# Kernel tuning notes

Measured on AMD Instinct MI355X. Metric: run time of the kernel, lower is better.

Reference implementation:

```python
import jax, jax.numpy as jnp
import numpy as np

D_MODEL = 1024
D_HIDDEN = 32   # per-head MPS bond dimension
N_HEADS = 8
D_FF = 4096
EPS_LN = 1e-5
EPS_NORM = 1e-6


def layernorm(x, g, b):
    m = jnp.mean(x, axis=-1, keepdims=True)
    v = jnp.mean(jnp.square(x - m), axis=-1, keepdims=True)
    return (x - m) * jax.lax.rsqrt(v + EPS_LN) * g + b


def mps_recurrence(x, Wa, ba, h0, Wo, bo):
    # x: [B,S,D]. Per-token per-head transfer matrices A_t in R^{dh x dh}.
    B, S, D = x.shape
    A = (x @ Wa + ba).reshape(B, S, N_HEADS, D_HIDDEN, D_HIDDEN)
    A = jnp.moveaxis(A, 1, 0)  # [S,B,H,dh,dh]
    h_init = jnp.broadcast_to(h0, (B, N_HEADS, D_HIDDEN))  # [B,H,dh]

    def step(h, A_t):
        h = jnp.einsum('bhij,bhj->bhi', A_t, h)
        h = h / (jnp.linalg.norm(h, axis=-1, keepdims=True) + EPS_NORM)
        return h, h

    _, ys = jax.lax.scan(step, h_init, A)          # ys: [S,B,H,dh]
    ys = jnp.moveaxis(ys, 0, 1).reshape(B, S, N_HEADS * D_HIDDEN)
    return ys @ Wo + bo                            # [B,S,D]


def setup_inputs() -> dict:
    key = jax.random.key(0)
    ks = jax.random.split(key, 12)
    B, S, D = 4, 2048, D_MODEL
    inv = 1.0 / np.sqrt(D)
    inv_hd = 1.0 / np.sqrt(N_HEADS * D_HIDDEN)
    return {
        'x': jax.random.normal(ks[0], (B, S, D), jnp.float32),
        'ln1_g': jnp.ones((D,), jnp.float32),
        'ln1_b': jnp.zeros((D,), jnp.float32),
        'Wa': jax.random.normal(ks[1], (D, N_HEADS * D_HIDDEN * D_HIDDEN), jnp.float32) * inv,
        'ba': jnp.zeros((N_HEADS * D_HIDDEN * D_HIDDEN,), jnp.float32),
        'h0': jax.random.normal(ks[2], (N_HEADS, D_HIDDEN), jnp.float32) / np.sqrt(D_HIDDEN),
        'Wo': jax.random.normal(ks[3], (N_HEADS * D_HIDDEN, D), jnp.float32) * inv_hd,
        'bo': jnp.zeros((D,), jnp.float32),
        'ln2_g': jnp.ones((D,), jnp.float32),
        'ln2_b': jnp.zeros((D,), jnp.float32),
        'W1': jax.random.normal(ks[4], (D, D_FF), jnp.float32) * inv,
        'b1': jnp.zeros((D_FF,), jnp.float32),
        'W2': jax.random.normal(ks[5], (D_FF, D), jnp.float32) / np.sqrt(D_FF),
        'b2': jnp.zeros((D,), jnp.float32),
    }


def reference(x, ln1_g, ln1_b, Wa, ba, h0, Wo, bo, ln2_g, ln2_b, W1, b1, W2, b2):
    # Dropout in eval mode (identity).
    x = x + mps_recurrence(layernorm(x, ln1_g, ln1_b), Wa, ba, h0, Wo, bo)
    h = layernorm(x, ln2_g, ln2_b)
    ffn = jax.nn.gelu(h @ W1 + b1, approximate=False) @ W2 + b2
    return x + ffn
```

## Files before the change

### kernel.cpp

```cpp
#include <hip/hip_runtime.h>
#include <hip/hip_bf16.h>
#include <math.h>

typedef float f32x4 __attribute__((ext_vector_type(4)));
typedef __bf16 bf16x4 __attribute__((ext_vector_type(4)));
typedef __bf16 bf16x8 __attribute__((ext_vector_type(8)));

#define AS1(p) ((const __attribute__((address_space(1))) void*)(p))
#define AS3(p) ((__attribute__((address_space(3))) void*)(p))

static constexpr int D_MODEL = 1024;
static constexpr int S_LEN   = 2048;
static constexpr int BATCH   = 4;
static constexpr int NTOK    = BATCH * S_LEN;
static constexpr int NH      = 8;
static constexpr int DH      = 32;
static constexpr int NA      = NH * DH * DH;
static constexpr int D_FF    = 4096;
static constexpr int CHUNK   = 16;
static constexpr int NCHUNK  = S_LEN / CHUNK;

__device__ __forceinline__ void xcd_swizzle(int& bx, int& by) {
  int gx = gridDim.x;
  int orig = by * gx + bx;
  int r8 = orig & 7, j = orig >> 3;
  int bxn = j % gx, grp = j / gx;
  bx = bxn;
  by = grp * 8 + r8;
}

__device__ __forceinline__ float gelu_erf_fast(float v) {
  float z = fabsf(v) * 0.70710678118654752f;
  float t = __builtin_amdgcn_rcpf(fmaf(0.3275911f, z, 1.0f));
  float p = t * (0.254829592f + t * (-0.284496736f + t * (1.421413741f +
            t * (-1.453152027f + t * 1.061405429f))));
  float e = __builtin_amdgcn_exp2f(-1.4426950408889634f * z * z);
  float er = 1.0f - p * e;
  er = (v < 0.0f) ? -er : er;
  return 0.5f * v * (1.0f + er);
}

__global__ __launch_bounds__(256) void transpose_bf16(
    const float* __restrict__ in, __bf16* __restrict__ out, int R, int C) {
  __shared__ float tile[32][33];
  int tx = threadIdx.x & 31, ty = threadIdx.x >> 5;
  int c0 = blockIdx.x * 32, r0 = blockIdx.y * 32;
  for (int i = ty; i < 32; i += 8)
    tile[i][tx] = in[(size_t)(r0 + i) * C + c0 + tx];
  __syncthreads();
  for (int i = ty; i < 32; i += 8)
    out[(size_t)(c0 + i) * R + r0 + tx] = (__bf16)tile[tx][i];
}

__global__ __launch_bounds__(256) void transpose_split(
    const float* __restrict__ in, __bf16* __restrict__ ohi,
    __bf16* __restrict__ olo, int R, int C) {
  __shared__ float tile[32][33];
  int tx = threadIdx.x & 31, ty = threadIdx.x >> 5;
  int c0 = blockIdx.x * 32, r0 = blockIdx.y * 32;
  for (int i = ty; i < 32; i += 8)
    tile[i][tx] = in[(size_t)(r0 + i) * C + c0 + tx];
  __syncthreads();
  for (int i = ty; i < 32; i += 8) {
    float v = tile[tx][i];
    __bf16 h = (__bf16)v;
    ohi[(size_t)(c0 + i) * R + r0 + tx] = h;
    olo[(size_t)(c0 + i) * R + r0 + tx] = (__bf16)(v - (float)h);
  }
}

template <int MODE>
__global__ __launch_bounds__(256) void ln_kernel(
    const float* __restrict__ in, const float* __restrict__ g,
    const float* __restrict__ bta, void* __restrict__ outv,
    void* __restrict__ outv2) {
  int row = blockIdx.x, tid = threadIdx.x;
  const float4* in4 = (const float4*)(in + (size_t)row * D_MODEL);
  float4 v = in4[tid];
  float s  = v.x + v.y + v.z + v.w;
  float ss = v.x * v.x + v.y * v.y + v.z * v.z + v.w * v.w;
  for (int o = 32; o; o >>= 1) { s += __shfl_down(s, o); ss += __shfl_down(ss, o); }
  __shared__ float ps[4], pq[4];
  int lane = tid & 63, w = tid >> 6;
  if (lane == 0) { ps[w] = s; pq[w] = ss; }
  __syncthreads();
  s  = ps[0] + ps[1] + ps[2] + ps[3];
  ss = pq[0] + pq[1] + pq[2] + pq[3];
  float mean = s * (1.0f / D_MODEL);
  float var  = ss * (1.0f / D_MODEL) - mean * mean;
  float inv  = rsqrtf(fmaxf(var, 0.0f) + 1e-5f);
  float4 gv = ((const float4*)g)[tid];
  float4 bv = ((const float4*)bta)[tid];
  float o0 = (v.x - mean) * inv * gv.x + bv.x;
  float o1 = (v.y - mean) * inv * gv.y + bv.y;
  float o2 = (v.z - mean) * inv * gv.z + bv.z;
  float o3 = (v.w - mean) * inv * gv.w + bv.w;
  if (MODE == 1) {
    float4 o = {o0, o1, o2, o3};
    ((float4*)outv)[(size_t)row * (D_MODEL / 4) + tid] = o;
  } else if (MODE == 0) {
    bf16x4 o;
    o[0] = (__bf16)o0; o[1] = (__bf16)o1; o[2] = (__bf16)o2; o[3] = (__bf16)o3;
    ((bf16x4*)outv)[(size_t)row * (D_MODEL / 4) + tid] = o;
  } else {
    bf16x4 oh, ol;
    oh[0] = (__bf16)o0; oh[1] = (__bf16)o1; oh[2] = (__bf16)o2; oh[3] = (__bf16)o3;
    ol[0] = (__bf16)(o0 - (float)oh[0]);
    ol[1] = (__bf16)(o1 - (float)oh[1]);
    ol[2] = (__bf16)(o2 - (float)oh[2]);
    ol[3] = (__bf16)(o3 - (float)oh[3]);
    ((bf16x4*)outv )[(size_t)row * (D_MODEL / 4) + tid] = oh;
    ((bf16x4*)outv2)[(size_t)row * (D_MODEL / 4) + tid] = ol;
  }
}

enum { EPI_BF16_BIAS = 0, EPI_BF16_BIAS_GELU = 1, EPI_F32_BIAS_RES = 2,
       EPI_F32_BIAS_ONLY = 3 };

#define SB0() __builtin_amdgcn_sched_barrier(0)
#define BARRIER()                                      \
  do {                                                 \
    SB0();                                             \
    __builtin_amdgcn_s_barrier();                      \
    SB0();                                             \
  } while (0)
#define LGKM0()                                        \
  do {                                                 \
    asm volatile("s_waitcnt lgkmcnt(0)" ::: "memory"); \
    SB0();                                             \
  } while (0)
#define GEMM8_QUAD(I0, J0)                                                   \
  do {                                                                       \
    __builtin_amdgcn_s_setprio(1);                                           \
    _Pragma("unroll") for (int i_ = 0; i_ < 4; ++i_)                         \
    _Pragma("unroll") for (int j_ = 0; j_ < 2; ++j_)                         \
    _Pragma("unroll") for (int k_ = 0; k_ < 2; ++k_)                         \
      acc[(I0) + i_][(J0) + j_] = __builtin_amdgcn_mfma_f32_16x16x32_bf16(   \
          a[(I0) + i_][k_], b[(J0) + j_][k_], acc[(I0) + i_][(J0) + j_],     \
          0, 0, 0);                                                          \
    __builtin_amdgcn_s_setprio(0);                                           \
  } while (0)

template <int SPLIT, int EPI>
__global__ __launch_bounds__(512, 2) void gemm8(
    const __bf16* __restrict__ pA, const __bf16* __restrict__ pA2,
    const __bf16* __restrict__ pB, const __bf16* __restrict__ pB2,
    const float* __restrict__ bias, void* __restrict__ out,
    int M, int N, int K) {
  __shared__ alignas(16) char lds[131072];
  const int tid = threadIdx.x;
  const int lane = tid & 63, w = tid >> 6;
  const int fm = lane & 15, fq = lane >> 4;
  const int wm2 = w >> 2, wn4 = w & 3;
  int bx = blockIdx.x, by = blockIdx.y;
  xcd_swizzle(bx, by);
  const int m0 = by * 256, n0 = bx * 256;
  const int NT = SPLIT ? 48 : (K >> 6);
  const int KS = SPLIT ? D_MODEL : K;

  const int lrow8 = lane >> 3;
  const int lslot = ((lane & 7) ^ lrow8) << 3;

  auto stageA = [&](int kt, int h) {
    const __bf16* base = SPLIT ? ((kt < 32) ? pA : pA2) : pA;
    int kc = SPLIT ? ((kt & 15) << 6) : (kt << 6);
    char* d0 = lds + ((kt & 1) << 15);
#pragma unroll
    for (int j = 0; j < 2; ++j) {
      int rb = h * 128 + j * 64 + w * 8;
      const __bf16* src = base + (size_t)(m0 + rb + lrow8) * KS + kc + lslot;
      __builtin_amdgcn_global_load_lds(AS1(src), AS3(d0 + rb * 128 + lane * 16), 16, 0, 0);
    }
  };
  auto stageB = [&](int kt, int h) {
    const __bf16* base = SPLIT ? ((kt >= 16 && kt < 32) ? pB2 : pB) : pB;
    int kc = SPLIT ? ((kt & 15) << 6) : (kt << 6);
    char* d0 = lds + 65536 + ((kt & 1) << 15);
#pragma unroll
    for (int j = 0; j < 2; ++j) {
      int rb = h * 128 + j * 64 + w * 8;
      const __bf16* src = base + (size_t)(n0 + rb + lrow8) * KS + kc + lslot;
      __builtin_amdgcn_global_load_lds(AS1(src), AS3(d0 + rb * 128 + lane * 16), 16, 0, 0);
    }
  };
  auto rdA = [&](int bo, int i, int ks) -> bf16x8 {
    int row = wm2 * 128 + i * 16 + fm;
    return *(const bf16x8*)(lds + bo + row * 128 +
                            ((((ks << 2) + fq) ^ (row & 7)) << 4));
  };
  auto rdB = [&](int bo, int j, int ks) -> bf16x8 {
    int row = wn4 * 64 + j * 16 + fm;
    return *(const bf16x8*)(lds + 65536 + bo + row * 128 +
                            ((((ks << 2) + fq) ^ (row & 7)) << 4));
  };

  f32x4 acc[8][4];
#pragma unroll
  for (int i = 0; i < 8; ++i)
#pragma unroll
    for (int j = 0; j < 4; ++j)
#pragma unroll
      for (int r = 0; r < 4; ++r) acc[i][j][r] = 0.0f;

  stageA(0, 0); stageA(0, 1); stageB(0, 0); stageB(0, 1);
  if (NT > 1) stageA(1, 0);
  SB0();
  if (NT > 1) asm volatile("s_waitcnt vmcnt(2)" ::: "memory");
  else        asm volatile("s_waitcnt vmcnt(0)" ::: "memory");
  BARRIER();
  bf16x8 a[8][2], b[4][2];
#pragma unroll
  for (int i = 0; i < 4; ++i) { a[i][0] = rdA(0, i, 0); a[i][1] = rdA(0, i, 1); }
#pragma unroll
  for (int j = 0; j < 2; ++j) { b[j][0] = rdB(0, j, 0); b[j][1] = rdB(0, j, 1); }

  for (int t = 0; t < NT; ++t) {
    const int bo  = (t & 1) << 15;
    const int bon = ((t + 1) & 1) << 15;
    BARRIER();
    if (t + 1 < NT) { stageA(t + 1, 1); stageB(t + 1, 0); }
    LGKM0();
#pragma unroll
    for (int j = 2; j < 4; ++j) { b[j][0] = rdB(bo, j, 0); b[j][1] = rdB(bo, j, 1); }
    SB0();
    GEMM8_QUAD(0, 0);
    BARRIER();
    if (t + 1 < NT) stageB(t + 1, 1);
    LGKM0();
#pragma unroll
    for (int i = 4; i < 8; ++i) { a[i][0] = rdA(bo, i, 0); a[i][1] = rdA(bo, i, 1); }
    SB0();
    GEMM8_QUAD(0, 2);
    BARRIER();
    LGKM0();
    GEMM8_QUAD(4, 0);
    BARRIER();
    if (t + 2 < NT) stageA(t + 2, 0);
    SB0();
    if (t + 1 < NT) {
      if (t + 2 < NT) asm volatile("s_waitcnt vmcnt(2)" ::: "memory");
      else            asm volatile("s_waitcnt vmcnt(0)" ::: "memory");
      BARRIER();
#pragma unroll
      for (int i = 0; i < 4; ++i) { a[i][0] = rdA(bon, i, 0); a[i][1] = rdA(bon, i, 1); }
#pragma unroll
      for (int j = 0; j < 2; ++j) { b[j][0] = rdB(bon, j, 0); b[j][1] = rdB(bon, j, 1); }
      SB0();
    }
    GEMM8_QUAD(4, 2);
  }
  __syncthreads();

  if (EPI == EPI_F32_BIAS_ONLY) {
    float* outF = (float*)out;
#pragma unroll
    for (int j = 0; j < 4; ++j) {
      int col = n0 + wn4 * 64 + j * 16 + fm;
      float bv = bias[col];
#pragma unroll
      for (int i = 0; i < 8; ++i)
#pragma unroll
        for (int r = 0; r < 4; ++r) {
          int row = m0 + wm2 * 128 + i * 16 + fq * 4 + r;
          outF[(size_t)row * N + col] = acc[i][j][r] + bv;
        }
    }
  } else {
    char* patch = lds + w * 16384;
    float bv4[4];
#pragma unroll
    for (int j = 0; j < 4; ++j) bv4[j] = bias[n0 + wn4 * 64 + j * 16 + fm];
#pragma unroll
    for (int i = 0; i < 8; ++i)
#pragma unroll
      for (int j = 0; j < 4; ++j)
#pragma unroll
        for (int r = 0; r < 4; ++r) {
          float v = gelu_erf_fast(acc[i][j][r] + bv4[j]);
          *(__bf16*)(patch + (i * 16 + fq * 4 + r) * 128 + (j * 16 + fm) * 2) =
              (__bf16)v;
        }
    asm volatile("s_waitcnt lgkmcnt(0)" ::: "memory");
#pragma unroll
    for (int rr = 0; rr < 16; ++rr) {
      bf16x8 ov = *(const bf16x8*)(patch + (rr * 8 + lrow8) * 128 + (lane & 7) * 16);
      size_t grow = (size_t)(m0 + wm2 * 128 + rr * 8 + lrow8);
      *(bf16x8*)((__bf16*)out + grow * N + n0 + wn4 * 64 + (lane & 7) * 8) = ov;
    }
  }
}

template <int EPI>
__global__ __launch_bounds__(256) void gemm_bf16(
    const __bf16* __restrict__ Amat, const __bf16* __restrict__ BT,
    const float* __restrict__ bias, const float* __restrict__ res,
    void* __restrict__ out, int M, int N, int K) {
  __shared__ __bf16 smem[2 * 128 * 32];
  __bf16* As = smem;
  __bf16* Bs = smem + 128 * 32;
  const int tid = threadIdx.x;
  const int lane = tid & 63, w = tid >> 6;
  int bx = blockIdx.x, by = blockIdx.y;
  xcd_swizzle(bx, by);
  const int m0 = by * 128, n0 = bx * 128;
  const int wm = (w >> 1) * 64, wn = (w & 1) * 64;

  f32x4 acc[4][4];
#pragma unroll
  for (int a = 0; a < 4; a++)
#pragma unroll
    for (int b = 0; b < 4; b++)
#pragma unroll
      for (int r = 0; r < 4; r++) acc[a][b][r] = 0.0f;

  const int srow = tid >> 2;
  const int soff = (tid & 3) * 16;
  const __bf16* gA0 = Amat + (size_t)(m0 + srow) * K + (soff >> 1);
  const __bf16* gA1 = Amat + (size_t)(m0 + srow + 64) * K + (soff >> 1);
  const __bf16* gB0 = BT + (size_t)(n0 + srow) * K + (soff >> 1);
  const __bf16* gB1 = BT + (size_t)(n0 + srow + 64) * K + (soff >> 1);
  char* lA0 = (char*)As + srow * 64 + soff;
  char* lA1 = (char*)As + (srow + 64) * 64 + soff;
  char* lB0 = (char*)Bs + srow * 64 + soff;
  char* lB1 = (char*)Bs + (srow + 64) * 64 + soff;

  const int fm = lane & 15, fq = lane >> 4;
  for (int k0 = 0; k0 < K; k0 += 32) {
    __builtin_amdgcn_global_load_lds(AS1(gA0 + k0), AS3(lA0), 16, 0, 0);
    __builtin_amdgcn_global_load_lds(AS1(gA1 + k0), AS3(lA1), 16, 0, 0);
    __builtin_amdgcn_global_load_lds(AS1(gB0 + k0), AS3(lB0), 16, 0, 0);
    __builtin_amdgcn_global_load_lds(AS1(gB1 + k0), AS3(lB1), 16, 0, 0);
    __syncthreads();
    bf16x8 af[4], bf[4];
#pragma unroll
    for (int t = 0; t < 4; t++)
      af[t] = *(const bf16x8*)((const char*)As + (wm + t * 16 + fm) * 64 + fq * 16);
#pragma unroll
    for (int t = 0; t < 4; t++)
      bf[t] = *(const bf16x8*)((const char*)Bs + (wn + t * 16 + fm) * 64 + fq * 16);
#pragma unroll
    for (int tm = 0; tm < 4; tm++)
#pragma unroll
      for (int tn = 0; tn < 4; tn++)
        acc[tm][tn] = __builtin_amdgcn_mfma_f32_16x16x32_bf16(af[tm], bf[tn], acc[tm][tn], 0, 0, 0);
    __syncthreads();
  }

#pragma unroll
  for (int tn = 0; tn < 4; tn++) {
    int col = n0 + wn + tn * 16 + fm;
    float bv = bias[col];
#pragma unroll
    for (int tm = 0; tm < 4; tm++) {
#pragma unroll
      for (int r = 0; r < 4; r++) {
        int row = m0 + wm + tm * 16 + fq * 4 + r;
        float v = acc[tm][tn][r] + bv;
        size_t idx = (size_t)row * N + col;
        if (EPI == EPI_F32_BIAS_RES) {
          ((float*)out)[idx] = v + res[idx];
        } else if (EPI == EPI_BF16_BIAS_GELU) {
          v = gelu_erf_fast(v);
          ((__bf16*)out)[idx] = (__bf16)v;
        } else {
          ((__bf16*)out)[idx] = (__bf16)v;
        }
      }
    }
  }
}

__global__ __launch_bounds__(64) void mps_chunkprod_f32(
    float* __restrict__ A) {
  int bid = blockIdx.x;
  int c = bid & 127, hh = bid >> 7;
  int lane = threadIdx.x;
  int jj = lane & 31, half = lane >> 5;
  __shared__ float Albuf[2][DH * DH];

  float curc[32];
#pragma unroll
  for (int k = 0; k < 32; k++) curc[k] = (k == jj) ? 1.0f : 0.0f;

  float* Abase = A + (size_t)(c * CHUNK) * NA + (size_t)hh * (DH * DH);

  {
    const float4* src = (const float4*)Abase;
    float4* dst = (float4*)Albuf[0];
#pragma unroll
    for (int r = 0; r < 4; r++) dst[lane + 64 * r] = src[lane + 64 * r];
  }
  __syncthreads();

  for (int t = 0; t < CHUNK; t++) {
    int cb = t & 1;
    float4 pf[4];
    if (t + 1 < CHUNK) {
      const float4* srcn = (const float4*)(Abase + (size_t)(t + 1) * NA);
#pragma unroll
      for (int r = 0; r < 4; r++) pf[r] = srcn[lane + 64 * r];
    }
    float nxt[16];
#pragma unroll
    for (int i16 = 0; i16 < 16; i16++) {
      const float4* ap = (const float4*)&Albuf[cb][(half * 16 + i16) * 32];
      float a0 = 0.f, a1 = 0.f, a2 = 0.f, a3 = 0.f;
#pragma unroll
      for (int k4 = 0; k4 < 8; k4++) {
        float4 av = ap[k4];
        a0 += av.x * curc[k4 * 4 + 0];
        a1 += av.y * curc[k4 * 4 + 1];
        a2 += av.z * curc[k4 * 4 + 2];
        a3 += av.w * curc[k4 * 4 + 3];
      }
      nxt[i16] = (a0 + a1) + (a2 + a3);
    }
    {
      float* slot = Abase + (size_t)t * NA;
#pragma unroll
      for (int i16 = 0; i16 < 16; i16++)
        slot[(half * 16 + i16) * 32 + jj] = nxt[i16];
    }
#pragma unroll
    for (int i16 = 0; i16 < 16; i16++) {
      float mine  = nxt[i16];
      float other = __shfl_xor(mine, 32);
      curc[i16]      = (half == 0) ? mine  : other;
      curc[16 + i16] = (half == 0) ? other : mine;
    }
    if (t + 1 < CHUNK) {
      float4* dst = (float4*)Albuf[cb ^ 1];
#pragma unroll
      for (int r = 0; r < 4; r++) dst[lane + 64 * r] = pf[r];
      __syncthreads();
    }
  }
}

__global__ __launch_bounds__(64) void mps_chunkscan(
    const float* __restrict__ pref, const float* __restrict__ h0,
    float* __restrict__ hstart) {
  int hh = blockIdx.x;
  int lane = threadIdx.x, i = lane & 31, half = lane >> 5;
  float hv = h0[hh * 32 + i];
  const size_t cstride = (size_t)CHUNK * NA;
  const float* row = pref + (size_t)(CHUNK - 1) * NA + (size_t)hh * (DH * DH)
                     + i * 32 + half * 16;
  int kb = half * 16;

  float4 pf0[4], pf1[4], pf2[4], pf3[4];
#pragma unroll
  for (int r = 0; r < 4; r++) pf0[r] = ((const float4*)row)[r];
#pragma unroll
  for (int r = 0; r < 4; r++) pf1[r] = ((const float4*)(row + cstride))[r];
#pragma unroll
  for (int r = 0; r < 4; r++) pf2[r] = ((const float4*)(row + 2 * cstride))[r];
#pragma unroll
  for (int r = 0; r < 4; r++) pf3[r] = ((const float4*)(row + 3 * cstride))[r];

  for (int c = 0; c < NCHUNK; c++) {
    if (lane < 32) hstart[((size_t)hh * NCHUNK + c) * 32 + i] = hv;
    float4 cur[4];
#pragma unroll
    for (int r = 0; r < 4; r++) cur[r] = pf0[r];
#pragma unroll
    for (int r = 0; r < 4; r++) pf0[r] = pf1[r];
#pragma unroll
    for (int r = 0; r < 4; r++) pf1[r] = pf2[r];
#pragma unroll
    for (int r = 0; r < 4; r++) pf2[r] = pf3[r];
    int cn = (c + 4 < NCHUNK) ? (c + 4) : (NCHUNK - 1);
#pragma unroll
    for (int r = 0; r < 4; r++)
      pf3[r] = ((const float4*)(row + (size_t)cn * cstride))[r];

    float a0 = 0.f, a1 = 0.f, a2 = 0.f, a3 = 0.f;
#pragma unroll
    for (int j4 = 0; j4 < 4; j4++) {
      float4 pv = cur[j4];
      a0 += pv.x * __shfl(hv, kb + j4 * 4 + 0);
      a1 += pv.y * __shfl(hv, kb + j4 * 4 + 1);
      a2 += pv.z * __shfl(hv, kb + j4 * 4 + 2);
      a3 += pv.w * __shfl(hv, kb + j4 * 4 + 3);
    }
    float y = (a0 + a1) + (a2 + a3);
    y += __shfl_xor(y, 32);
    float nn = y * y;
#pragma unroll
    for (int o = 16; o; o >>= 1) nn += __shfl_xor(nn, o);
    hv = y / (sqrtf(nn) + 1e-6f);
  }
}

__global__ __launch_bounds__(256) void mps_expand_par(
    const float* __restrict__ pref, const float* __restrict__ hstart,
    __bf16* __restrict__ ys, int tok0base) {
  int w = threadIdx.x >> 6, lane = threadIdx.x & 63;
  int i = lane & 31, half = lane >> 5;
  int task = blockIdx.x * 4 + w;
  int hh = task & 7, tok = task >> 3;
  int c = tok >> 4, t = tok & 15;
  int kb = half * 16;

  if (t == CHUNK - 1 && c < NCHUNK - 1) {
    if (lane < 32) {
      float hv2 = hstart[((size_t)hh * NCHUNK + c + 1) * 32 + i];
      ys[(size_t)(tok0base + tok) * (NH * DH) + hh * 32 + i] = (__bf16)hv2;
    }
    return;
  }

  float hv = hstart[((size_t)hh * NCHUNK + c) * 32 + i];
  const float4* Mr = (const float4*)(pref + (size_t)tok * NA
                     + (size_t)hh * (DH * DH) + i * 32 + half * 16);
  float4 m0 = Mr[0], m1 = Mr[1], m2 = Mr[2], m3 = Mr[3];

  float a0 = 0.f, a1 = 0.f, a2 = 0.f, a3 = 0.f;
  a0 += m0.x * __shfl(hv, kb + 0);  a1 += m0.y * __shfl(hv, kb + 1);
  a2 += m0.z * __shfl(hv, kb + 2);  a3 += m0.w * __shfl(hv, kb + 3);
  a0 += m1.x * __shfl(hv, kb + 4);  a1 += m1.y * __shfl(hv, kb + 5);
  a2 += m1.z * __shfl(hv, kb + 6);  a3 += m1.w * __shfl(hv, kb + 7);
  a0 += m2.x * __shfl(hv, kb + 8);  a1 += m2.y * __shfl(hv, kb + 9);
  a2 += m2.z * __shfl(hv, kb + 10); a3 += m2.w * __shfl(hv, kb + 11);
  a0 += m3.x * __shfl(hv, kb + 12); a1 += m3.y * __shfl(hv, kb + 13);
  a2 += m3.z * __shfl(hv, kb + 14); a3 += m3.w * __shfl(hv, kb + 15);
  float y = (a0 + a1) + (a2 + a3);
  y += __shfl_xor(y, 32);
  float nn = y * y;
#pragma unroll
  for (int o = 16; o; o >>= 1) nn += __shfl_xor(nn, o);
  float hvo = y / (sqrtf(nn) + 1e-6f);
  if (lane < 32)
    ys[(size_t)(tok0base + tok) * (NH * DH) + hh * 32 + i] = (__bf16)hvo;
}

extern "C" void kernel_launch(void* const* d_in, const int* in_sizes, int n_in,
                              void* d_out, int out_size, void* d_ws, size_t ws_size,
                              hipStream_t stream) {
  const float* x     = (const float*)d_in[0];
  const float* ln1_g = (const float*)d_in[1];
  const float* ln1_b = (const float*)d_in[2];
  const float* Wa    = (const float*)d_in[3];
  const float* ba    = (const float*)d_in[4];
  const float* h0    = (const float*)d_in[5];
  const float* Wo    = (const float*)d_in[6];
  const float* bo    = (const float*)d_in[7];
  const float* ln2_g = (const float*)d_in[8];
  const float* ln2_b = (const float*)d_in[9];
  const float* W1    = (const float*)d_in[10];
  const float* b1    = (const float*)d_in[11];
  const float* W2    = (const float*)d_in[12];
  const float* b2    = (const float*)d_in[13];
  float* out = (float*)d_out;

  char* wsb = (char*)d_ws;
  size_t off = 0;
  auto alloc = [&](size_t bytes) -> void* {
    void* p = wsb + off;
    off += (bytes + 255) & ~(size_t)255;
    return p;
  };
  __bf16* WoT   = (__bf16*)alloc((size_t)(NH * DH) * D_MODEL * 2);
  __bf16* W1T   = (__bf16*)alloc((size_t)D_MODEL * D_FF * 2);
  __bf16* W2T   = (__bf16*)alloc((size_t)D_FF * D_MODEL * 2);
  __bf16* ys    = (__bf16*)alloc((size_t)NTOK * NH * DH * 2);
  float*  hst   = (float*) alloc((size_t)NH * NCHUNK * DH * 4);
  __bf16* xnh   = (__bf16*)alloc((size_t)NTOK * D_MODEL * 2);
  __bf16* xnl   = (__bf16*)alloc((size_t)NTOK * D_MODEL * 2);
  __bf16* WaTh  = (__bf16*)alloc((size_t)D_MODEL * NA * 2);
  __bf16* WaTl  = (__bf16*)alloc((size_t)D_MODEL * NA * 2);
  size_t tail0 = off;
  float*  Af32 = (float*) alloc((size_t)S_LEN * NA * 4);
  __bf16* mid  = (__bf16*)(wsb + tail0);

  transpose_bf16<<<dim3(D_MODEL / 32, (NH * DH) / 32), 256, 0, stream>>>(Wo, WoT, NH * DH, D_MODEL);
  transpose_bf16<<<dim3(D_FF / 32, D_MODEL / 32), 256, 0, stream>>>(W1, W1T, D_MODEL, D_FF);
  transpose_bf16<<<dim3(D_MODEL / 32, D_FF / 32), 256, 0, stream>>>(W2, W2T, D_FF, D_MODEL);
  transpose_split<<<dim3(NA / 32, D_MODEL / 32), 256, 0, stream>>>(Wa, WaTh, WaTl, D_MODEL, NA);

  ln_kernel<2><<<NTOK, 256, 0, stream>>>(x, ln1_g, ln1_b, xnh, xnl);

  for (int b = 0; b < BATCH; b++) {
    gemm8<1, EPI_F32_BIAS_ONLY><<<dim3(NA / 256, S_LEN / 256), 512, 0, stream>>>(
        xnh + (size_t)b * S_LEN * D_MODEL, xnl + (size_t)b * S_LEN * D_MODEL,
        WaTh, WaTl, ba, Af32, S_LEN, NA, D_MODEL);
    mps_chunkprod_f32<<<NH * NCHUNK, 64, 0, stream>>>(Af32);
    mps_chunkscan<<<NH, 64, 0, stream>>>(Af32, h0, hst);
    mps_expand_par<<<(S_LEN * NH) / 4, 256, 0, stream>>>(Af32, hst, ys, b * S_LEN);
  }

  gemm_bf16<EPI_F32_BIAS_RES><<<dim3(D_MODEL / 128, NTOK / 128), 256, 0, stream>>>(
      ys, WoT, bo, x, out, NTOK, D_MODEL, NH * DH);

  ln_kernel<0><<<NTOK, 256, 0, stream>>>(out, ln2_g, ln2_b, xnh, nullptr);

  gemm8<0, EPI_BF16_BIAS_GELU><<<dim3(D_FF / 256, NTOK / 256), 512, 0, stream>>>(
      xnh, nullptr, W1T, nullptr, b1, mid, NTOK, D_FF, D_MODEL);

  gemm_bf16<EPI_F32_BIAS_RES><<<dim3(D_MODEL / 128, NTOK / 128), 256, 0, stream>>>(
      mid, W2T, b2, out, out, NTOK, D_MODEL, D_FF);
}
```

Before: 1.395 ms.

## Run FFN down-projection on 256x256 MFMA kernel with split-K atomic accumulation

Replaces the 128x128 gemm_bf16 used for the W2 projection with the larger 256x256 gemm8 kernel, split two ways along K (grid z=2) and accumulated into the fp32 output with atomicAdd; only the first split adds the bias, and the residual comes from the existing contents of out. This targets the long K=4096 GEMM and gives the 4x32 tile grid enough blocks. It also adds a launch_bounds occupancy hint of 3 to gemm_bf16. Per-element fp32 atomics add memory traffic and make the summation order nondeterministic.

```diff
diff --git a/kernel.cpp b/kernel.cpp
--- a/kernel.cpp
+++ b/kernel.cpp
@@ -115,7 +115,7 @@
 }
 
 enum { EPI_BF16_BIAS = 0, EPI_BF16_BIAS_GELU = 1, EPI_F32_BIAS_RES = 2,
-       EPI_F32_BIAS_ONLY = 3 };
+       EPI_F32_BIAS_ONLY = 3, EPI_F32_ATOMIC = 4 };
 
 #define SB0() __builtin_amdgcn_sched_barrier(0)
 #define BARRIER()                                      \
@@ -141,12 +141,12 @@
     __builtin_amdgcn_s_setprio(0);                                           \
   } while (0)
 
-template <int SPLIT, int EPI>
+template <int SPLIT, int SPLITK, int EPI>
 __global__ __launch_bounds__(512, 2) void gemm8(
     const __bf16* __restrict__ pA, const __bf16* __restrict__ pA2,
     const __bf16* __restrict__ pB, const __bf16* __restrict__ pB2,
     const float* __restrict__ bias, void* __restrict__ out,
-    int M, int N, int K) {
+    int M, int N, int K, int kstride) {
   __shared__ alignas(16) char lds[131072];
   const int tid = threadIdx.x;
   const int lane = tid & 63, w = tid >> 6;
@@ -156,13 +156,17 @@
   xcd_swizzle(bx, by);
   const int m0 = by * 256, n0 = bx * 256;
   const int NT = SPLIT ? 48 : (K >> 6);
-  const int KS = SPLIT ? D_MODEL : K;
+  const int KS = SPLIT ? D_MODEL : kstride;
+
+  const size_t kzoff = SPLITK ? (size_t)blockIdx.z * (size_t)K : 0;
+  const __bf16* pAz = pA + kzoff;
+  const __bf16* pBz = pB + kzoff;
 
   const int lrow8 = lane >> 3;
   const int lslot = ((lane & 7) ^ lrow8) << 3;
 
   auto stageA = [&](int kt, int h) {
-    const __bf16* base = SPLIT ? ((kt < 32) ? pA : pA2) : pA;
+    const __bf16* base = SPLIT ? ((kt < 32) ? pA : pA2) : pAz;
     int kc = SPLIT ? ((kt & 15) << 6) : (kt << 6);
     char* d0 = lds + ((kt & 1) << 15);
 #pragma unroll
@@ -173,7 +177,7 @@
     }
   };
   auto stageB = [&](int kt, int h) {
-    const __bf16* base = SPLIT ? ((kt >= 16 && kt < 32) ? pB2 : pB) : pB;
+    const __bf16* base = SPLIT ? ((kt >= 16 && kt < 32) ? pB2 : pB) : pBz;
     int kc = SPLIT ? ((kt & 15) << 6) : (kt << 6);
     char* d0 = lds + 65536 + ((kt & 1) << 15);
 #pragma unroll
@@ -265,6 +269,20 @@
           outF[(size_t)row * N + col] = acc[i][j][r] + bv;
         }
     }
+  } else if (EPI == EPI_F32_ATOMIC) {
+    float* outF = (float*)out;
+#pragma unroll
+    for (int j = 0; j < 4; ++j) {
+      int col = n0 + wn4 * 64 + j * 16 + fm;
+      float bv = (blockIdx.z == 0) ? bias[col] : 0.0f;
+#pragma unroll
+      for (int i = 0; i < 8; ++i)
+#pragma unroll
+        for (int r = 0; r < 4; ++r) {
+          int row = m0 + wm2 * 128 + i * 16 + fq * 4 + r;
+          atomicAdd(&outF[(size_t)row * N + col], acc[i][j][r] + bv);
+        }
+    }
   } else {
     char* patch = lds + w * 16384;
     float bv4[4];
@@ -291,7 +309,7 @@
 }
 
 template <int EPI>
-__global__ __launch_bounds__(256) void gemm_bf16(
+__global__ __launch_bounds__(256, 3) void gemm_bf16(
     const __bf16* __restrict__ Amat, const __bf16* __restrict__ BT,
     const float* __restrict__ bias, const float* __restrict__ res,
     void* __restrict__ out, int M, int N, int K) {
@@ -581,9 +599,9 @@
   ln_kernel<2><<<NTOK, 256, 0, stream>>>(x, ln1_g, ln1_b, xnh, xnl);
 
   for (int b = 0; b < BATCH; b++) {
-    gemm8<1, EPI_F32_BIAS_ONLY><<<dim3(NA / 256, S_LEN / 256), 512, 0, stream>>>(
+    gemm8<1, 0, EPI_F32_BIAS_ONLY><<<dim3(NA / 256, S_LEN / 256), 512, 0, stream>>>(
         xnh + (size_t)b * S_LEN * D_MODEL, xnl + (size_t)b * S_LEN * D_MODEL,
-        WaTh, WaTl, ba, Af32, S_LEN, NA, D_MODEL);
+        WaTh, WaTl, ba, Af32, S_LEN, NA, D_MODEL, D_MODEL);
     mps_chunkprod_f32<<<NH * NCHUNK, 64, 0, stream>>>(Af32);
     mps_chunkscan<<<NH, 64, 0, stream>>>(Af32, h0, hst);
     mps_expand_par<<<(S_LEN * NH) / 4, 256, 0, stream>>>(Af32, hst, ys, b * S_LEN);
@@ -594,9 +612,9 @@
 
   ln_kernel<0><<<NTOK, 256, 0, stream>>>(out, ln2_g, ln2_b, xnh, nullptr);
 
-  gemm8<0, EPI_BF16_BIAS_GELU><<<dim3(D_FF / 256, NTOK / 256), 512, 0, stream>>>(
-      xnh, nullptr, W1T, nullptr, b1, mid, NTOK, D_FF, D_MODEL);
-
-  gemm_bf16<EPI_F32_BIAS_RES><<<dim3(D_MODEL / 128, NTOK / 128), 256, 0, stream>>>(
-      mid, W2T, b2, out, out, NTOK, D_MODEL, D_FF);
-}
+  gemm8<0, 0, EPI_BF16_BIAS_GELU><<<dim3(D_FF / 256, NTOK / 256), 512, 0, stream>>>(
+      xnh, nullptr, W1T, nullptr, b1, mid, NTOK, D_FF, D_MODEL, D_MODEL);
+
+  gemm8<0, 1, EPI_F32_ATOMIC><<<dim3(D_MODEL / 256, NTOK / 256, 2), 512, 0, stream>>>(
+      mid, nullptr, W2T, nullptr, b2, out, NTOK, D_MODEL, D_FF / 2, D_FF);
+}
```

Result: no change. 1.404 ms (+0.6%).
